# Kernel tuning notes

Hardware: AMD Instinct MI355X
Metric: run time of the kernel (lower is better)

## Reference

```python
import jax, jax.numpy as jnp
import numpy as np

N_EXPERT = 64
EMBD_DIM = 4096
TOP_K = 8
NEG_INF = -1e30  # stand-in for -inf, safe in fp16/bf16 softmax


def setup_inputs() -> dict:
    key = jax.random.key(0)
    kx, kw = jax.random.split(key)
    x = jax.random.normal(kx, (4, 4096, EMBD_DIM), dtype=jnp.float32)
    # nn.Linear weight: [out_features, in_features] = [n_expert, embd_dim]
    W = jax.random.normal(kw, (N_EXPERT, EMBD_DIM), dtype=jnp.float32) / np.sqrt(EMBD_DIM)
    return {"x": x, "W": W}


def reference(x, W):
    # logits = x @ W^T : [b, s, e]
    logits = jnp.einsum('bsd,ed->bse', x, W)
    top_k_logits, indices = jax.lax.top_k(logits, TOP_K)  # [b,s,k]
    # scatter top-k logits into a -inf tensor == keep logits where selected, -inf elsewhere
    mask = jnp.any(indices[..., None] == jnp.arange(N_EXPERT), axis=-2)  # [b,s,e] bool
    masked = jnp.where(mask, logits, NEG_INF)
    probs = jax.nn.softmax(masked, axis=-1)
    return probs, indices
```

## Files before the change

kernel.cpp:

```cpp
#include <hip/hip_runtime.h>
#include <math.h>

#define TOKENS 16384
#define EMBD   4096
#define NEXP   64
#define TOPK   8
#define KSPLIT 8
#define KSLICE (EMBD / KSPLIT)
#define CHUNK  16

__global__ void transpose_w(const float* __restrict__ W, float* __restrict__ Wt) {
    int idx = blockIdx.x * blockDim.x + threadIdx.x;
    int e = idx >> 12;
    int k = idx & 4095;
    Wt[k * NEXP + e] = W[idx];
}

__global__ __launch_bounds__(256, 2) void gemm_partial(
    const float* __restrict__ x, const float* __restrict__ Wt,
    float* __restrict__ part) {
    const int lane = threadIdx.x & 63;
    const int wave = threadIdx.x >> 6;
    const int tok  = blockIdx.x * 256 + wave * 64 + lane;
    const int ks   = blockIdx.y;
    const int kbase = ks * KSLICE;

    const float* xrow = x + (size_t)tok * EMBD + kbase;

    double accd[NEXP];
#pragma unroll
    for (int e = 0; e < NEXP; ++e) accd[e] = 0.0;

    for (int kc = 0; kc < KSLICE; kc += CHUNK) {
        const float4* xp = (const float4*)(xrow + kc);
        float4 a = xp[0], b = xp[1], c = xp[2], d4 = xp[3];
        float xv[CHUNK] = {a.x, a.y, a.z, a.w,  b.x, b.y, b.z, b.w,
                           c.x, c.y, c.z, c.w,  d4.x, d4.y, d4.z, d4.w};

        float accf[NEXP];
#pragma unroll
        for (int e = 0; e < NEXP; ++e) accf[e] = 0.0f;

#pragma unroll
        for (int j = 0; j < CHUNK; ++j) {
            const float xj = xv[j];
            const float* wrow = Wt + (size_t)(kbase + kc + j) * NEXP;
#pragma unroll
            for (int e = 0; e < NEXP; ++e)
                accf[e] = fmaf(wrow[e], xj, accf[e]);
        }

#pragma unroll
        for (int e = 0; e < NEXP; ++e) accd[e] += (double)accf[e];
    }

    float* dst = part + ((size_t)ks * TOKENS + tok) * NEXP;
#pragma unroll
    for (int e = 0; e < NEXP; ++e) dst[e] = (float)accd[e];
}

__global__ __launch_bounds__(256) void topk_softmax(
    const float* __restrict__ part, float* __restrict__ probs,
    float* __restrict__ idxout) {
    const int lane = threadIdx.x & 63;
    const int wave = threadIdx.x >> 6;
    const int tok  = blockIdx.x * 4 + wave;

    double d = 0.0;
#pragma unroll
    for (int s = 0; s < KSPLIT; ++s)
        d += (double)part[((size_t)s * TOKENS + tok) * NEXP + lane];
    const float logit = (float)d;

    float v = logit;
    float m = 0.0f, denom = 0.0f;
    int myidx = 0;
    unsigned long long selmask = 0ull;

    for (int r = 0; r < TOPK; ++r) {
        float bv = v;
        int   bi = lane;
#pragma unroll
        for (int off = 32; off > 0; off >>= 1) {
            float ov = __shfl_xor(bv, off);
            int   oi = __shfl_xor(bi, off);
            if (ov > bv || (ov == bv && oi < bi)) { bv = ov; bi = oi; }
        }
        if (r == 0) m = bv;
        denom += expf(bv - m);
        selmask |= 1ull << bi;
        if (lane == r) myidx = bi;
        if (lane == bi) v = -INFINITY;
    }

    const float p = ((selmask >> lane) & 1ull) ? (expf(logit - m) / denom) : 0.0f;
    probs[(size_t)tok * NEXP + lane] = p;
    if (lane < TOPK) idxout[(size_t)tok * TOPK + lane] = (float)myidx;
}

extern "C" void kernel_launch(void* const* d_in, const int* in_sizes, int n_in,
                              void* d_out, int out_size, void* d_ws, size_t ws_size,
                              hipStream_t stream) {
    const float* x = (const float*)d_in[0];
    const float* W = (const float*)d_in[1];

    float* out    = (float*)d_out;
    float* probs  = out;
    float* idxout = out + (size_t)TOKENS * NEXP;

    float* Wt   = (float*)d_ws;
    float* part = Wt + (size_t)EMBD * NEXP;

    hipLaunchKernelGGL(transpose_w, dim3((EMBD * NEXP) / 256), dim3(256), 0, stream,
                       W, Wt);
    hipLaunchKernelGGL(gemm_partial, dim3(TOKENS / 256, KSPLIT), dim3(256), 0, stream,
                       x, Wt, part);
    hipLaunchKernelGGL(topk_softmax, dim3(TOKENS / 4), dim3(256), 0, stream,
                       part, probs, idxout);
}
```

Measured before the change: 535.6 us.

## Split expert dimension across wave pairs in GEMM and rank-based top-k

The GEMM kernel now has each pair of waves share 64 tokens, with each wave computing half the experts. This halves the per-thread accumulator registers and raises the launch-bounds occupancy target from 2 to 3, at the cost of loading each x row twice. Partial results are written as float4 stores. The top-k kernel replaces eight serial shuffle-reduction rounds with a per-lane rank count over logits staged in shared memory, plus a single shuffle reduction for the softmax denominator.

Measured after the change: 436.2 us. -18.6%, faster.

```diff
diff --git a/kernel.cpp b/kernel.cpp
--- a/kernel.cpp
+++ b/kernel.cpp
@@ -8,6 +8,7 @@
 #define KSPLIT 8
 #define KSLICE (EMBD / KSPLIT)
 #define CHUNK  16
+#define EHALF  32
 
 __global__ void transpose_w(const float* __restrict__ W, float* __restrict__ Wt) {
     int idx = blockIdx.x * blockDim.x + threadIdx.x;
@@ -16,20 +17,23 @@
     Wt[k * NEXP + e] = W[idx];
 }
 
-__global__ __launch_bounds__(256, 2) void gemm_partial(
+__global__ __launch_bounds__(256, 3) void gemm_partial(
     const float* __restrict__ x, const float* __restrict__ Wt,
     float* __restrict__ part) {
     const int lane = threadIdx.x & 63;
     const int wave = threadIdx.x >> 6;
-    const int tok  = blockIdx.x * 256 + wave * 64 + lane;
+    const int tgrp = wave >> 1;
+    const int half = __builtin_amdgcn_readfirstlane(wave & 1);
+    const int tok  = blockIdx.x * 128 + tgrp * 64 + lane;
     const int ks   = blockIdx.y;
     const int kbase = ks * KSLICE;
 
-    const float* xrow = x + (size_t)tok * EMBD + kbase;
+    const float* xrow  = x + (size_t)tok * EMBD + kbase;
+    const float* wbase = Wt + (size_t)kbase * NEXP + half * EHALF;
 
-    double accd[NEXP];
+    double accd[EHALF];
 #pragma unroll
-    for (int e = 0; e < NEXP; ++e) accd[e] = 0.0;
+    for (int e = 0; e < EHALF; ++e) accd[e] = 0.0;
 
     for (int kc = 0; kc < KSLICE; kc += CHUNK) {
         const float4* xp = (const float4*)(xrow + kc);
@@ -37,31 +41,37 @@
         float xv[CHUNK] = {a.x, a.y, a.z, a.w,  b.x, b.y, b.z, b.w,
                            c.x, c.y, c.z, c.w,  d4.x, d4.y, d4.z, d4.w};
 
-        float accf[NEXP];
+        float accf[EHALF];
 #pragma unroll
-        for (int e = 0; e < NEXP; ++e) accf[e] = 0.0f;
+        for (int e = 0; e < EHALF; ++e) accf[e] = 0.0f;
 
 #pragma unroll
         for (int j = 0; j < CHUNK; ++j) {
             const float xj = xv[j];
-            const float* wrow = Wt + (size_t)(kbase + kc + j) * NEXP;
+            const float* wrow = wbase + (size_t)(kc + j) * NEXP;
 #pragma unroll
-            for (int e = 0; e < NEXP; ++e)
+            for (int e = 0; e < EHALF; ++e)
                 accf[e] = fmaf(wrow[e], xj, accf[e]);
         }
 
 #pragma unroll
-        for (int e = 0; e < NEXP; ++e) accd[e] += (double)accf[e];
+        for (int e = 0; e < EHALF; ++e) accd[e] += (double)accf[e];
     }
 
-    float* dst = part + ((size_t)ks * TOKENS + tok) * NEXP;
+    float4* dst = (float4*)(part + ((size_t)ks * TOKENS + tok) * NEXP
+                            + (size_t)half * EHALF);
 #pragma unroll
-    for (int e = 0; e < NEXP; ++e) dst[e] = (float)accd[e];
+    for (int v = 0; v < EHALF / 4; ++v)
+        dst[v] = make_float4((float)accd[4 * v],     (float)accd[4 * v + 1],
+                             (float)accd[4 * v + 2], (float)accd[4 * v + 3]);
 }
 
 __global__ __launch_bounds__(256) void topk_softmax(
     const float* __restrict__ part, float* __restrict__ probs,
     float* __restrict__ idxout) {
+    __shared__ float lval[4][NEXP];
+    __shared__ float lidx[4][TOPK];
+
     const int lane = threadIdx.x & 63;
     const int wave = threadIdx.x >> 6;
     const int tok  = blockIdx.x * 4 + wave;
@@ -72,30 +82,36 @@
         d += (double)part[((size_t)s * TOKENS + tok) * NEXP + lane];
     const float logit = (float)d;
 
-    float v = logit;
-    float m = 0.0f, denom = 0.0f;
-    int myidx = 0;
-    unsigned long long selmask = 0ull;
+    lval[wave][lane] = logit;
+    __syncthreads();
 
-    for (int r = 0; r < TOPK; ++r) {
-        float bv = v;
-        int   bi = lane;
+    const float4* lv4 = (const float4*)lval[wave];
+    int rank = 0;
+    float m = -INFINITY;
 #pragma unroll
-        for (int off = 32; off > 0; off >>= 1) {
-            float ov = __shfl_xor(bv, off);
-            int   oi = __shfl_xor(bi, off);
-            if (ov > bv || (ov == bv && oi < bi)) { bv = ov; bi = oi; }
-        }
-        if (r == 0) m = bv;
-        denom += expf(bv - m);
-        selmask |= 1ull << bi;
-        if (lane == r) myidx = bi;
-        if (lane == bi) v = -INFINITY;
+    for (int q4 = 0; q4 < NEXP / 4; ++q4) {
+        float4 v = lv4[q4];
+        const int qb = q4 * 4;
+        rank += (v.x > logit || (v.x == logit && qb + 0 < lane)) ? 1 : 0;
+        rank += (v.y > logit || (v.y == logit && qb + 1 < lane)) ? 1 : 0;
+        rank += (v.z > logit || (v.z == logit && qb + 2 < lane)) ? 1 : 0;
+        rank += (v.w > logit || (v.w == logit && qb + 3 < lane)) ? 1 : 0;
+        m = fmaxf(fmaxf(m, v.x), fmaxf(v.y, fmaxf(v.z, v.w)));
     }
 
-    const float p = ((selmask >> lane) & 1ull) ? (expf(logit - m) / denom) : 0.0f;
-    probs[(size_t)tok * NEXP + lane] = p;
-    if (lane < TOPK) idxout[(size_t)tok * TOPK + lane] = (float)myidx;
+    const bool sel = rank < TOPK;
+    const float t  = sel ? expf(logit - m) : 0.0f;
+
+    float denom = t;
+#pragma unroll
+    for (int off = 32; off > 0; off >>= 1)
+        denom += __shfl_xor(denom, off);
+
+    if (sel) lidx[wave][rank] = (float)lane;
+    __syncthreads();
+
+    probs[(size_t)tok * NEXP + lane] = sel ? (t / denom) : 0.0f;
+    if (lane < TOPK) idxout[(size_t)tok * TOPK + lane] = lidx[wave][lane];
 }
 
 extern "C" void kernel_launch(void* const* d_in, const int* in_sizes, int n_in,
@@ -113,7 +129,7 @@
 
     hipLaunchKernelGGL(transpose_w, dim3((EMBD * NEXP) / 256), dim3(256), 0, stream,
                        W, Wt);
-    hipLaunchKernelGGL(gemm_partial, dim3(TOKENS / 256, KSPLIT), dim3(256), 0, stream,
+    hipLaunchKernelGGL(gemm_partial, dim3(TOKENS / 128, KSPLIT), dim3(256), 0, stream,
                        x, Wt, part);
     hipLaunchKernelGGL(topk_softmax, dim3(TOKENS / 4), dim3(256), 0, stream,
                        part, probs, idxout);
```
